# Optimization experiments

Measured on AMD Instinct MI355X. Metric: run time of the kernel, lower is better.

Reference implementation:

```python
import jax, jax.numpy as jnp
import numpy as np

B, P, M, C = 64, 8732, 16, 81
THRESHOLD = 0.5
NEG_POS_RATIO = 3
ALPHA = 1.0  # config.reg_weights
EPS = 1e-7


def cxcy_to_xy(c):
    return jnp.concatenate([c[..., :2] - c[..., 2:] / 2.0,
                            c[..., :2] + c[..., 2:] / 2.0], axis=-1)


def _rand_boxes_cxcy(key, shape):
    k1, k2 = jax.random.split(key)
    cxcy = jax.random.uniform(k1, shape + (2,), minval=0.2, maxval=0.8)
    wh = jax.random.uniform(k2, shape + (2,), minval=0.05, maxval=0.35)
    return jnp.concatenate([cxcy, wh], axis=-1)


def setup_inputs() -> dict:
    key = jax.random.key(0)
    ks = jax.random.split(key, 5)
    predicted_locs = cxcy_to_xy(_rand_boxes_cxcy(ks[0], (B, P)))          # valid corner boxes
    predicted_scores = jax.random.normal(ks[1], (B, P, C), dtype=jnp.float32)
    boxes = jnp.clip(cxcy_to_xy(_rand_boxes_cxcy(ks[2], (B, M))), 0.0, 1.0)  # GT corner boxes
    labels = jax.random.randint(ks[3], (B, M), 1, C)                       # object labels (1..C-1)
    priors_cxcy = _rand_boxes_cxcy(ks[4], (P,))
    return {"predicted_locs": predicted_locs, "predicted_scores": predicted_scores,
            "boxes": boxes, "labels": labels, "priors_cxcy": priors_cxcy}


def jaccard(a, b):
    # a: [M,4], b: [P,4] corner boxes -> [M,P] IoU
    lt = jnp.maximum(a[:, None, :2], b[None, :, :2])
    rb = jnp.minimum(a[:, None, 2:], b[None, :, 2:])
    wh = jnp.clip(rb - lt, 0.0)
    inter = wh[..., 0] * wh[..., 1]
    area_a = (a[:, 2] - a[:, 0]) * (a[:, 3] - a[:, 1])
    area_b = (b[:, 2] - b[:, 0]) * (b[:, 3] - b[:, 1])
    return inter / (area_a[:, None] + area_b[None, :] - inter)


def diou_loss(b1, b2):
    # corner boxes, elementwise over leading dims -> per-box loss 1 - DIoU
    lt = jnp.maximum(b1[..., :2], b2[..., :2])
    rb = jnp.minimum(b1[..., 2:], b2[..., 2:])
    wh = jnp.clip(rb - lt, 0.0)
    inter = wh[..., 0] * wh[..., 1]
    area1 = (b1[..., 2] - b1[..., 0]) * (b1[..., 3] - b1[..., 1])
    area2 = (b2[..., 2] - b2[..., 0]) * (b2[..., 3] - b2[..., 1])
    iou = inter / (area1 + area2 - inter + EPS)
    c1 = (b1[..., :2] + b1[..., 2:]) / 2.0
    c2 = (b2[..., :2] + b2[..., 2:]) / 2.0
    inter_diag = jnp.sum((c1 - c2) ** 2, axis=-1)
    enc_lt = jnp.minimum(b1[..., :2], b2[..., :2])
    enc_rb = jnp.maximum(b1[..., 2:], b2[..., 2:])
    outer_diag = jnp.sum((enc_rb - enc_lt) ** 2, axis=-1)
    dious = jnp.clip(iou - inter_diag / (outer_diag + EPS), -1.0, 1.0)
    return 1.0 - dious


def reference(predicted_locs, predicted_scores, boxes, labels, priors_cxcy):
    priors_xy = cxcy_to_xy(priors_cxcy)

    def assign(boxes_i, labels_i):
        overlap = jaccard(boxes_i, priors_xy)              # [M, P]
        ovl_prior = overlap.max(axis=0)                    # best overlap per prior
        obj_prior = overlap.argmax(axis=0)                 # best object per prior
        ovl_obj = overlap.max(axis=1)                      # best overlap per object
        prior_obj = overlap.argmax(axis=1)                 # best prior per object
        valid = ovl_obj > 0
        j_idx = jnp.cumsum(valid.astype(jnp.int32)) - 1    # index within filtered list (faithful)
        idx = jnp.where(valid, prior_obj, P)               # P -> dropped (out of bounds)
        ovl_prior = ovl_prior.at[idx].set(1.0, mode='drop')
        obj_prior = obj_prior.at[idx].set(j_idx, mode='drop')
        lab = labels_i[obj_prior]
        label_pos = jnp.where(ovl_prior < THRESHOLD, 0, lab)
        label_neg = jnp.where(ovl_prior < THRESHOLD - 0.1, -1, lab)
        return label_pos, label_neg

    true_classes, true_neg_classes = jax.vmap(assign)(boxes, labels)  # [B,P] each
    positive = true_classes > 0                                        # [B,P]
    pos_f = positive.astype(jnp.float32)
    n_pos_total = jnp.sum(pos_f)

    # Localization loss: DIoU(pred_pos, pred_pos) with reduce='mean' (faithful to source)
    per_box = diou_loss(predicted_locs, predicted_locs)                # [B,P]
    loc_loss = jnp.sum(per_box * pos_f) / jnp.maximum(n_pos_total, 1.0)

    # Confidence loss: per-prior CE + hard-negative mining (neg_pos_ratio)
    logp = jax.nn.log_softmax(predicted_scores, axis=-1)
    conf_all = -jnp.take_along_axis(logp, true_classes[..., None], axis=-1)[..., 0]  # [B,P]
    conf_pos_sum = jnp.sum(conf_all * pos_f)
    conf_neg = jnp.where(positive, 0.0, conf_all)
    conf_neg_sorted = -jnp.sort(-conf_neg, axis=-1)                    # descending
    n_hard = NEG_POS_RATIO * jnp.sum(positive, axis=1)                 # [B]
    hard_mask = (jnp.arange(P)[None, :] < n_hard[:, None]).astype(jnp.float32)
    conf_loss = (jnp.sum(conf_neg_sorted * hard_mask) + conf_pos_sum) / n_pos_total

    return conf_loss + ALPHA * loc_loss
```

## Files before the change

### kernel.cpp

```cpp
#include <hip/hip_runtime.h>
#include <math.h>

#define B_ 64
#define P_ 8732
#define M_ 16
#define C_ 81
#define THRESH 0.5f
#define EPS_ 1e-7f

#define TILE_ 128
#define NBLK_CE ((B_ * P_) / TILE_)

__global__ __launch_bounds__(1024) void assign_kernel(
    const float* __restrict__ boxes,
    const int*   __restrict__ labels,
    const float* __restrict__ priors,
    int*         __restrict__ true_classes,
    int*         __restrict__ n_pos)
{
    const int b = blockIdx.x;
    const int tid = threadIdx.x;
    const int lane = tid & 63;
    const int wv = tid >> 6;

    __shared__ float s_ovl[P_];
    __shared__ unsigned char s_obj[P_];
    __shared__ float s_bx[M_][4];
    __shared__ float s_barea[M_];
    __shared__ int   s_lab[M_];
    __shared__ float s_wv[M_][16];
    __shared__ int   s_wp[M_][16];
    __shared__ float s_ovl_obj[M_];
    __shared__ int   s_prior_obj[M_];
    __shared__ int   s_cnt[16];

    if (tid < M_*4) ((float*)s_bx)[tid] = boxes[b*M_*4 + tid];
    if (tid < M_)   s_lab[tid] = labels[b*M_ + tid];
    __syncthreads();
    if (tid < M_)
        s_barea[tid] = (s_bx[tid][2]-s_bx[tid][0])*(s_bx[tid][3]-s_bx[tid][1]);
    __syncthreads();

    float bestv[M_]; int bestp[M_];
    #pragma unroll
    for (int m = 0; m < M_; ++m) { bestv[m] = -1.0f; bestp[m] = 0x7fffffff; }

    for (int p = tid; p < P_; p += 1024) {
        float4 pc = ((const float4*)priors)[p];
        float px1 = pc.x - pc.z*0.5f, py1 = pc.y - pc.w*0.5f;
        float px2 = pc.x + pc.z*0.5f, py2 = pc.y + pc.w*0.5f;
        float parea = (px2-px1)*(py2-py1);
        float bv = -1.0f; int bm = 0;
        #pragma unroll
        for (int m = 0; m < M_; ++m) {
            float ix1 = fmaxf(s_bx[m][0], px1);
            float iy1 = fmaxf(s_bx[m][1], py1);
            float ix2 = fminf(s_bx[m][2], px2);
            float iy2 = fminf(s_bx[m][3], py2);
            float iw = fmaxf(ix2-ix1, 0.0f);
            float ih = fmaxf(iy2-iy1, 0.0f);
            float inter = iw*ih;
            float iou = inter / (s_barea[m] + parea - inter);
            if (iou > bv) { bv = iou; bm = m; }
            if (iou > bestv[m]) { bestv[m] = iou; bestp[m] = p; }
        }
        s_ovl[p] = bv;
        s_obj[p] = (unsigned char)bm;
    }

    #pragma unroll
    for (int m = 0; m < M_; ++m) {
        float v = bestv[m]; int p = bestp[m];
        #pragma unroll
        for (int o = 32; o; o >>= 1) {
            float v2 = __shfl_xor(v, o);
            int   p2 = __shfl_xor(p, o);
            if (v2 > v || (v2 == v && p2 < p)) { v = v2; p = p2; }
        }
        if (lane == 0) { s_wv[m][wv] = v; s_wp[m][wv] = p; }
    }
    __syncthreads();

    if (tid < M_) {
        float v = s_wv[tid][0]; int p = s_wp[tid][0];
        #pragma unroll
        for (int w = 1; w < 16; ++w) {
            float v2 = s_wv[tid][w]; int p2 = s_wp[tid][w];
            if (v2 > v || (v2 == v && p2 < p)) { v = v2; p = p2; }
        }
        s_ovl_obj[tid] = v; s_prior_obj[tid] = p;
    }
    __syncthreads();

    if (tid == 0) {
        int cnt = 0;
        for (int m = 0; m < M_; ++m) {
            if (s_ovl_obj[m] > 0.0f) {
                int p = s_prior_obj[m];
                s_ovl[p] = 1.0f;
                s_obj[p] = (unsigned char)cnt;
                cnt++;
            }
        }
    }
    __syncthreads();

    int cpos = 0;
    for (int p = tid; p < P_; p += 1024) {
        int tc = 0;
        if (!(s_ovl[p] < THRESH)) tc = s_lab[s_obj[p]];
        true_classes[(size_t)b*P_ + p] = tc;
        cpos += (tc > 0);
    }
    #pragma unroll
    for (int o = 32; o; o >>= 1) cpos += __shfl_xor(cpos, o);
    if (lane == 0) s_cnt[wv] = cpos;
    __syncthreads();
    if (tid == 0) {
        int t = 0;
        #pragma unroll
        for (int w = 0; w < 16; ++w) t += s_cnt[w];
        n_pos[b] = t;
    }
}

__global__ __launch_bounds__(128) void ce_loc_kernel(
    const float* __restrict__ scores,
    const float* __restrict__ locs,
    const int*   __restrict__ tcls,
    float*       __restrict__ conf_neg,
    float*       __restrict__ blk_pos,
    float*       __restrict__ blk_loc)
{
    __shared__ float s[TILE_ * C_];
    __shared__ float s_red[2][2];
    const int tid = threadIdx.x;
    const int tile = blockIdx.x;

    const float4* g4 = (const float4*)(scores + (size_t)tile * TILE_ * C_);
    float4* s4 = (float4*)s;
    #pragma unroll 4
    for (int i = tid; i < TILE_*C_/4; i += TILE_) s4[i] = g4[i];
    __syncthreads();

    const float* row = s + tid * C_;
    float mx = row[0];
    #pragma unroll 8
    for (int c = 1; c < C_; ++c) mx = fmaxf(mx, row[c]);
    float e = 0.f;
    #pragma unroll 8
    for (int c = 0; c < C_; ++c) e += __expf(row[c] - mx);

    const int r = tile * TILE_ + tid;
    const int t = tcls[r];
    float conf = mx + __logf(e) - row[t];

    float p = 0.f, l = 0.f;
    if (t > 0) {
        conf_neg[r] = 0.f;
        p = conf;
        float4 bx = ((const float4*)locs)[r];
        float w = bx.z - bx.x, h = bx.w - bx.y;
        float iw = fmaxf(w, 0.f), ih = fmaxf(h, 0.f);
        float inter = iw * ih;
        float area  = w * h;
        float iou   = inter / (area + area - inter + EPS_);
        float diou  = fminf(fmaxf(iou, -1.f), 1.f);
        l = 1.f - diou;
    } else {
        conf_neg[r] = fmaxf(conf, 0.f);
    }

    #pragma unroll
    for (int o = 32; o; o >>= 1) { p += __shfl_xor(p, o); l += __shfl_xor(l, o); }
    if ((tid & 63) == 0) { s_red[tid >> 6][0] = p; s_red[tid >> 6][1] = l; }
    __syncthreads();
    if (tid == 0) {
        blk_pos[tile] = s_red[0][0] + s_red[1][0];
        blk_loc[tile] = s_red[0][1] + s_red[1][1];
    }
}

__global__ __launch_bounds__(1024) void topk_kernel(
    const float* __restrict__ conf_neg,
    const int*   __restrict__ n_pos,
    float*       __restrict__ hard)
{
    const int b = blockIdx.x;
    const int tid = threadIdx.x;
    const int lane = tid & 63;
    const int wv = tid >> 6;
    __shared__ float s_v[P_];
    __shared__ int   s_t[16];
    __shared__ float s_f[16];
    __shared__ int   s_bcast;

    for (int i = tid; i < P_; i += 1024) s_v[i] = conf_neg[(size_t)b*P_ + i];
    int k = 3 * n_pos[b];
    if (k <= 0) { if (tid == 0) hard[b] = 0.f; return; }
    if (k > P_) k = P_;
    __syncthreads();

    unsigned prefix = 0u;
    for (int bit = 30; bit >= 0; --bit) {
        unsigned cand = prefix | (1u << bit);
        int c = 0;
        for (int i = tid; i < P_; i += 1024)
            c += (__float_as_uint(s_v[i]) >= cand) ? 1 : 0;
        #pragma unroll
        for (int o = 32; o; o >>= 1) c += __shfl_xor(c, o);
        if (lane == 0) s_t[wv] = c;
        __syncthreads();
        if (tid == 0) {
            int tot = 0;
            #pragma unroll
            for (int w = 0; w < 16; ++w) tot += s_t[w];
            s_bcast = tot;
        }
        __syncthreads();
        if (s_bcast >= k) prefix = cand;
        __syncthreads();
    }
    float tval = __uint_as_float(prefix);

    float sum = 0.f; int cgt = 0;
    for (int i = tid; i < P_; i += 1024) {
        float v = s_v[i];
        if (v > tval) { sum += v; cgt++; }
    }
    #pragma unroll
    for (int o = 32; o; o >>= 1) { sum += __shfl_xor(sum, o); cgt += __shfl_xor(cgt, o); }
    if (lane == 0) { s_f[wv] = sum; s_t[wv] = cgt; }
    __syncthreads();
    if (tid == 0) {
        float s = 0.f; int c = 0;
        #pragma unroll
        for (int w = 0; w < 16; ++w) { s += s_f[w]; c += s_t[w]; }
        hard[b] = s + (float)(k - c) * tval;
    }
}

__global__ __launch_bounds__(256) void final_kernel(
    const float* __restrict__ blk_pos,
    const float* __restrict__ blk_loc,
    const float* __restrict__ hard,
    const int*   __restrict__ n_pos,
    float*       __restrict__ out)
{
    const int tid = threadIdx.x;
    const int lane = tid & 63;
    const int wv = tid >> 6;
    __shared__ double sd[4][4];

    double p = 0.0, l = 0.0, h = 0.0, np = 0.0;
    for (int i = tid; i < NBLK_CE; i += 256) { p += blk_pos[i]; l += blk_loc[i]; }
    if (tid < B_) { h = hard[tid]; np = (double)n_pos[tid]; }

    #pragma unroll
    for (int o = 32; o; o >>= 1) {
        p += __shfl_xor(p, o); l += __shfl_xor(l, o);
        h += __shfl_xor(h, o); np += __shfl_xor(np, o);
    }
    if (lane == 0) { sd[wv][0] = p; sd[wv][1] = l; sd[wv][2] = h; sd[wv][3] = np; }
    __syncthreads();
    if (tid == 0) {
        double tp = 0, tl = 0, th = 0, tn = 0;
        #pragma unroll
        for (int w = 0; w < 4; ++w) { tp += sd[w][0]; tl += sd[w][1]; th += sd[w][2]; tn += sd[w][3]; }
        double conf_loss = (th + tp) / tn;
        double loc_loss  = tl / fmax(tn, 1.0);
        out[0] = (float)(conf_loss + 1.0 * loc_loss);
    }
}

extern "C" void kernel_launch(void* const* d_in, const int* in_sizes, int n_in,
                              void* d_out, int out_size, void* d_ws, size_t ws_size,
                              hipStream_t stream) {
    const float* predicted_locs   = (const float*)d_in[0];
    const float* predicted_scores = (const float*)d_in[1];
    const float* boxes            = (const float*)d_in[2];
    const int*   labels           = (const int*)d_in[3];
    const float* priors           = (const float*)d_in[4];
    float* out = (float*)d_out;

    char* ws = (char*)d_ws;
    size_t off = 0;
    int*    true_classes = (int*)(ws + off);   off += sizeof(int)   * (size_t)B_ * P_;
    float*  conf_neg     = (float*)(ws + off); off += sizeof(float) * (size_t)B_ * P_;
    int*    n_pos        = (int*)(ws + off);   off += sizeof(int)   * B_;
    float*  hard         = (float*)(ws + off); off += sizeof(float) * B_;
    float*  blk_pos      = (float*)(ws + off); off += sizeof(float) * NBLK_CE;
    float*  blk_loc      = (float*)(ws + off); off += sizeof(float) * NBLK_CE;

    assign_kernel<<<B_, 1024, 0, stream>>>(boxes, labels, priors,
                                           true_classes, n_pos);
    ce_loc_kernel<<<NBLK_CE, TILE_, 0, stream>>>(predicted_scores, predicted_locs,
                                                 true_classes, conf_neg,
                                                 blk_pos, blk_loc);
    topk_kernel<<<B_, 1024, 0, stream>>>(conf_neg, n_pos, hard);
    final_kernel<<<1, 256, 0, stream>>>(blk_pos, blk_loc, hard, n_pos, out);
}
```

Before: 392.1 us.

## Use 16-lane groups per row in CE kernel and radix-histogram top-k selection

The cross-entropy kernel no longer stages a 128-row tile in shared memory with one thread per row. Each wavefront now handles four rows at a time, sixteen lanes per row, reading scores straight from global memory in a grid-stride loop and reducing max, sum-exp and the target logit with shuffles. The top-k threshold search replaces the 31-pass bitwise count with a 4-round 8-bit radix histogram using per-wave shared-memory atomics and a prefix scan. The aim is better parallelism and memory coalescing in CE and far fewer block-wide barriers in top-k, at the cost of shared-memory atomic contention and more complex selection logic.

```diff
diff --git a/kernel.cpp b/kernel.cpp
--- a/kernel.cpp
+++ b/kernel.cpp
@@ -8,8 +8,8 @@
 #define THRESH 0.5f
 #define EPS_ 1e-7f
 
-#define TILE_ 128
-#define NBLK_CE ((B_ * P_) / TILE_)
+#define CE_BLOCKS 2048
+#define NBLK_CE CE_BLOCKS
 
 __global__ __launch_bounds__(1024) void assign_kernel(
     const float* __restrict__ boxes,
@@ -124,7 +124,7 @@
     }
 }
 
-__global__ __launch_bounds__(128) void ce_loc_kernel(
+__global__ __launch_bounds__(256) void ce_loc_kernel(
     const float* __restrict__ scores,
     const float* __restrict__ locs,
     const int*   __restrict__ tcls,
@@ -132,52 +132,76 @@
     float*       __restrict__ blk_pos,
     float*       __restrict__ blk_loc)
 {
-    __shared__ float s[TILE_ * C_];
-    __shared__ float s_red[2][2];
-    const int tid = threadIdx.x;
-    const int tile = blockIdx.x;
-
-    const float4* g4 = (const float4*)(scores + (size_t)tile * TILE_ * C_);
-    float4* s4 = (float4*)s;
-    #pragma unroll 4
-    for (int i = tid; i < TILE_*C_/4; i += TILE_) s4[i] = g4[i];
-    __syncthreads();
-
-    const float* row = s + tid * C_;
-    float mx = row[0];
-    #pragma unroll 8
-    for (int c = 1; c < C_; ++c) mx = fmaxf(mx, row[c]);
-    float e = 0.f;
-    #pragma unroll 8
-    for (int c = 0; c < C_; ++c) e += __expf(row[c] - mx);
-
-    const int r = tile * TILE_ + tid;
-    const int t = tcls[r];
-    float conf = mx + __logf(e) - row[t];
-
-    float p = 0.f, l = 0.f;
-    if (t > 0) {
-        conf_neg[r] = 0.f;
-        p = conf;
-        float4 bx = ((const float4*)locs)[r];
-        float w = bx.z - bx.x, h = bx.w - bx.y;
-        float iw = fmaxf(w, 0.f), ih = fmaxf(h, 0.f);
-        float inter = iw * ih;
-        float area  = w * h;
-        float iou   = inter / (area + area - inter + EPS_);
-        float diou  = fminf(fmaxf(iou, -1.f), 1.f);
-        l = 1.f - diou;
-    } else {
-        conf_neg[r] = fmaxf(conf, 0.f);
-    }
-
-    #pragma unroll
-    for (int o = 32; o; o >>= 1) { p += __shfl_xor(p, o); l += __shfl_xor(l, o); }
-    if ((tid & 63) == 0) { s_red[tid >> 6][0] = p; s_red[tid >> 6][1] = l; }
-    __syncthreads();
-    if (tid == 0) {
-        blk_pos[tile] = s_red[0][0] + s_red[1][0];
-        blk_loc[tile] = s_red[0][1] + s_red[1][1];
+    const int tid  = threadIdx.x;
+    const int lane = tid & 63;
+    const int j    = lane & 15;
+    const int g    = lane >> 4;
+    const int wv   = tid >> 6;
+    const int gwave = blockIdx.x * 4 + wv;
+    const int ngrp  = CE_BLOCKS * 4;
+    const int NG = (B_ * P_) / 4;
+
+    __shared__ float s_red[4][2];
+
+    float p_acc = 0.f, l_acc = 0.f;
+
+    for (int grp = gwave; grp < NG; grp += ngrp) {
+        const int r = grp * 4 + g;
+        const float* row = scores + (size_t)r * C_;
+
+        float x[6];
+        #pragma unroll
+        for (int k = 0; k < 5; ++k) x[k] = row[16*k + j];
+        x[5] = (j == 0) ? row[80] : -INFINITY;
+
+        float mx = fmaxf(fmaxf(fmaxf(x[0], x[1]), fmaxf(x[2], x[3])),
+                         fmaxf(x[4], x[5]));
+        #pragma unroll
+        for (int o = 1; o < 16; o <<= 1) mx = fmaxf(mx, __shfl_xor(mx, o));
+
+        const int t = tcls[r];
+        float e = 0.f, st = 0.f;
+        #pragma unroll
+        for (int k = 0; k < 6; ++k) {
+            e += __expf(x[k] - mx);
+            const int idx = 16*k + j;
+            if (idx == t) st = x[k];
+        }
+        #pragma unroll
+        for (int o = 1; o < 16; o <<= 1) {
+            e  += __shfl_xor(e, o);
+            st += __shfl_xor(st, o);
+        }
+
+        if (j == 0) {
+            float conf = mx + __logf(e) - st;
+            if (t > 0) {
+                conf_neg[r] = 0.f;
+                p_acc += conf;
+                float4 bx = ((const float4*)locs)[r];
+                float w = bx.z - bx.x, h = bx.w - bx.y;
+                float iw = fmaxf(w, 0.f), ih = fmaxf(h, 0.f);
+                float inter = iw * ih;
+                float area  = w * h;
+                float iou   = inter / (area + area - inter + EPS_);
+                float diou  = fminf(fmaxf(iou, -1.f), 1.f);
+                l_acc += 1.f - diou;
+            } else {
+                conf_neg[r] = fmaxf(conf, 0.f);
+            }
+        }
+    }
+
+    #pragma unroll
+    for (int o = 32; o; o >>= 1) {
+        p_acc += __shfl_xor(p_acc, o);
+        l_acc += __shfl_xor(l_acc, o);
+    }
+    if (lane == 0) { s_red[wv][0] = p_acc; s_red[wv][1] = l_acc; }
+    __syncthreads();
+    if (tid == 0) {
+        blk_pos[blockIdx.x] = s_red[0][0] + s_red[1][0] + s_red[2][0] + s_red[3][0];
+        blk_loc[blockIdx.x] = s_red[0][1] + s_red[1][1] + s_red[2][1] + s_red[3][1];
     }
 }
 
@@ -190,10 +214,13 @@
     const int tid = threadIdx.x;
     const int lane = tid & 63;
     const int wv = tid >> 6;
+
     __shared__ float s_v[P_];
+    __shared__ int   s_hist[16][256];
+    __shared__ int   s_cg[257];
+    __shared__ int   s_sel;
     __shared__ int   s_t[16];
     __shared__ float s_f[16];
-    __shared__ int   s_bcast;
 
     for (int i = tid; i < P_; i += 1024) s_v[i] = conf_neg[(size_t)b*P_ + i];
     int k = 3 * n_pos[b];
@@ -201,27 +228,61 @@
     if (k > P_) k = P_;
     __syncthreads();
 
+    const unsigned masks[4]  = {0u, 0xFF800000u, 0xFFFF8000u, 0xFFFFFF80u};
+    const int      shifts[4] = {23, 15, 7, 0};
+
     unsigned prefix = 0u;
-    for (int bit = 30; bit >= 0; --bit) {
-        unsigned cand = prefix | (1u << bit);
-        int c = 0;
-        for (int i = tid; i < P_; i += 1024)
-            c += (__float_as_uint(s_v[i]) >= cand) ? 1 : 0;
-        #pragma unroll
-        for (int o = 32; o; o >>= 1) c += __shfl_xor(c, o);
-        if (lane == 0) s_t[wv] = c;
-        __syncthreads();
-        if (tid == 0) {
-            int tot = 0;
-            #pragma unroll
-            for (int w = 0; w < 16; ++w) tot += s_t[w];
-            s_bcast = tot;
-        }
-        __syncthreads();
-        if (s_bcast >= k) prefix = cand;
-        __syncthreads();
-    }
-    float tval = __uint_as_float(prefix);
+    int k_rem = k;
+
+    for (int rd = 0; rd < 4; ++rd) {
+        const unsigned hm = masks[rd];
+        const int sh = shifts[rd];
+
+        ((int*)s_hist)[tid] = 0;
+        ((int*)s_hist)[tid + 1024] = 0;
+        ((int*)s_hist)[tid + 2048] = 0;
+        ((int*)s_hist)[tid + 3072] = 0;
+        __syncthreads();
+
+        for (int i = tid; i < P_; i += 1024) {
+            unsigned u = __float_as_uint(s_v[i]);
+            if ((u & hm) == prefix)
+                atomicAdd(&s_hist[wv][(u >> sh) & 0xFF], 1);
+        }
+        __syncthreads();
+
+        if (wv == 0) {
+            int carry = 0;
+            for (int c = 3; c >= 0; --c) {
+                int bin = c * 64 + lane;
+                int tot = 0;
+                #pragma unroll
+                for (int w = 0; w < 16; ++w) tot += s_hist[w][bin];
+                #pragma unroll
+                for (int o = 1; o < 64; o <<= 1) {
+                    int v = __shfl_down(tot, o);
+                    if (lane + o < 64) tot += v;
+                }
+                int cg = tot + carry;
+                s_cg[bin] = cg;
+                carry = __shfl(cg, 0);
+            }
+            if (lane == 0) s_cg[256] = 0;
+        }
+        __syncthreads();
+
+        if (tid < 256) {
+            if (s_cg[tid] >= k_rem && s_cg[tid + 1] < k_rem) s_sel = tid;
+        }
+        __syncthreads();
+
+        const int bsel = s_sel;
+        k_rem -= s_cg[bsel + 1];
+        prefix |= (unsigned)bsel << sh;
+        __syncthreads();
+    }
+
+    const float tval = __uint_as_float(prefix);
 
     float sum = 0.f; int cgt = 0;
     for (int i = tid; i < P_; i += 1024) {
@@ -294,7 +355,7 @@
 
     assign_kernel<<<B_, 1024, 0, stream>>>(boxes, labels, priors,
                                            true_classes, n_pos);
-    ce_loc_kernel<<<NBLK_CE, TILE_, 0, stream>>>(predicted_scores, predicted_locs,
+    ce_loc_kernel<<<CE_BLOCKS, 256, 0, stream>>>(predicted_scores, predicted_locs,
                                                  true_classes, conf_neg,
                                                  blk_pos, blk_loc);
     topk_kernel<<<B_, 1024, 0, stream>>>(conf_neg, n_pos, hard);
```

Result: faster. 359.4 us (-8.3%).
